# Performance work log

Measured on AMD Instinct MI355X. Metric: run time of the kernel, lower is better.

The kernel has to match this reference:

```python
import jax, jax.numpy as jnp
import numpy as np

# dims
B_, L_, DIN, H, DOUT, NL = 2, 1024, 512, 768, 512, 4
ED, N, K = H, 16, 4            # expand_factor=1 -> d_inner=H; d_state=16; d_conv=4
DTR = (H + 15) // 16           # dt_rank = ceil(d_model/16) = 48


def setup_inputs() -> dict:
    key = jax.random.key(0)
    ks = iter(jax.random.split(key, 32))
    def g(shape, s=0.02):
        return jax.random.normal(next(ks), shape, jnp.float32) * s
    inp = dict(
        x=jax.random.normal(next(ks), (B_, L_, DIN), jnp.float32),
        in_proj_w=g((H, DIN)), in_proj_b=jnp.zeros((H,), jnp.float32),
        out_proj_w=g((DOUT, H)), out_proj_b=jnp.zeros((DOUT,), jnp.float32),
        ln1_w=jnp.ones((NL, H), jnp.float32), ln1_b=jnp.zeros((NL, H), jnp.float32),
        ln2_w=jnp.ones((NL, H), jnp.float32), ln2_b=jnp.zeros((NL, H), jnp.float32),
        ffn_w1=g((NL, 4 * H, H)), ffn_b1=jnp.zeros((NL, 4 * H), jnp.float32),
        ffn_w2=g((NL, H, 4 * H)), ffn_b2=jnp.zeros((NL, H), jnp.float32),
        rms_w=jnp.ones((NL, ED), jnp.float32),
        m_in_w=g((NL, 2 * ED, H)),
        conv_w=g((NL, ED, 1, K), 0.2), conv_b=jnp.zeros((NL, ED), jnp.float32),
        xproj_w=g((NL, DTR + 2 * N, ED)),
        dt_w=g((NL, ED, DTR), 0.1), dt_b=g((NL, ED), 0.1),
        A_log=jnp.log(jnp.tile(jnp.arange(1, N + 1, dtype=jnp.float32), (NL, ED, 1))),
        Dp=jnp.ones((NL, ED), jnp.float32),
        m_out_w=g((NL, H, ED)),
    )
    return inp


def _layernorm(x, w, b):
    m = x.mean(-1, keepdims=True)
    v = ((x - m) ** 2).mean(-1, keepdims=True)
    return (x - m) / jnp.sqrt(v + 1e-5) * w + b


def _rmsnorm(x, w):
    return x * jax.lax.rsqrt((x * x).mean(-1, keepdims=True) + 1e-5) * w


def _selective_scan(dA, dBx):
    # h_t = dA_t * h_{t-1} + dBx_t, done as a parallel associative scan over L
    def comb(c1, c2):
        a1, b1 = c1
        a2, b2 = c2
        return a1 * a2, a2 * b1 + b2
    _, h = jax.lax.associative_scan(comb, (dA, dBx), axis=1)
    return h  # (B, L, ED, N)


def _mamba(x, rw, iw, cw, cb, xw, dw, db, Alog, Dp, ow):
    # mambapy ResidualBlock: x + MambaBlock(RMSNorm(x))
    xn = _rmsnorm(x, rw)
    xz = xn @ iw.T                             # (B, L, 2*ED)
    xi, z = jnp.split(xz, 2, axis=-1)
    # causal depthwise conv1d (padding = K-1 left)
    xc = jax.lax.conv_general_dilated(
        xi.transpose(0, 2, 1), cw, (1,), [(K - 1, 0)],
        feature_group_count=ED, dimension_numbers=('NCH', 'OIH', 'NCH'))
    xi = jax.nn.silu(xc.transpose(0, 2, 1) + cb)
    dbc = xi @ xw.T                            # (B, L, DTR + 2N)
    d = dbc[..., :DTR]
    Bm = dbc[..., DTR:DTR + N]
    Cm = dbc[..., DTR + N:]
    delta = jax.nn.softplus(d @ dw.T + db)     # (B, L, ED)
    A = -jnp.exp(Alog)                         # (ED, N)
    dA = jnp.exp(delta[..., None] * A)         # (B, L, ED, N)
    dBx = (delta * xi)[..., None] * Bm[:, :, None, :]
    h = _selective_scan(dA, dBx)
    y = jnp.einsum('blen,bln->ble', h, Cm) + Dp * xi
    y = y * jax.nn.silu(z)
    return x + y @ ow.T


def reference(x, in_proj_w, in_proj_b, out_proj_w, out_proj_b,
              ln1_w, ln1_b, ln2_w, ln2_b,
              ffn_w1, ffn_b1, ffn_w2, ffn_b2,
              rms_w, m_in_w, conv_w, conv_b, xproj_w,
              dt_w, dt_b, A_log, Dp, m_out_w):
    h = x @ in_proj_w.T + in_proj_b
    for i in range(NL):
        h = h + _mamba(_layernorm(h, ln1_w[i], ln1_b[i]),
                       rms_w[i], m_in_w[i], conv_w[i], conv_b[i], xproj_w[i],
                       dt_w[i], dt_b[i], A_log[i], Dp[i], m_out_w[i])
        hn = _layernorm(h, ln2_w[i], ln2_b[i])
        h = h + jax.nn.relu(hn @ ffn_w1[i].T + ffn_b1[i]) @ ffn_w2[i].T + ffn_b2[i]
    return h @ out_proj_w.T + out_proj_b
```

## Files before the change

### kernel.cpp

```cpp
#include <hip/hip_runtime.h>
#include <stdint.h>

typedef unsigned short u16;
typedef __attribute__((ext_vector_type(8))) short short8;
typedef __attribute__((ext_vector_type(4))) float f32x4;

static __device__ __forceinline__ u16 f2bf(float f){
  unsigned int x = __float_as_uint(f);
  unsigned int r = (x + 0x7FFFu + ((x >> 16) & 1u)) >> 16;
  return (u16)r;
}
static __device__ __forceinline__ float bf2f(u16 u){
  return __uint_as_float(((unsigned int)u) << 16);
}

__global__ __launch_bounds__(256) void prep_cvt(
    const float* __restrict__ s0, const float* __restrict__ s1,
    const float* __restrict__ s2, const float* __restrict__ s3,
    const float* __restrict__ s4, const float* __restrict__ s5,
    const float* __restrict__ s6,
    u16* __restrict__ d0, u16* __restrict__ d1, u16* __restrict__ d2,
    u16* __restrict__ d3, u16* __restrict__ d4, u16* __restrict__ d5,
    u16* __restrict__ d6){
  size_t i = ((size_t)blockIdx.x * 256 + threadIdx.x) * 4;
  const float* src; u16* dst; size_t base;
  if      (i <  1048576){ src = s0; dst = d0; base = 0; }
  else if (i <  1441792){ src = s1; dst = d1; base = 1048576; }
  else if (i <  1835008){ src = s2; dst = d2; base = 1441792; }
  else if (i <  6553600){ src = s3; dst = d3; base = 1835008; }
  else if (i <  8912896){ src = s4; dst = d4; base = 6553600; }
  else if (i < 18350080){ src = s5; dst = d5; base = 8912896; }
  else                  { src = s6; dst = d6; base = 18350080; }
  size_t o = i - base;
  float4 v = *reinterpret_cast<const float4*>(src + o);
  union { u16 u[4]; unsigned long long ll; } t;
  t.u[0] = f2bf(v.x); t.u[1] = f2bf(v.y); t.u[2] = f2bf(v.z); t.u[3] = f2bf(v.w);
  *reinterpret_cast<unsigned long long*>(dst + o) = t.ll;
}

__global__ __launch_bounds__(256) void build_dbc(const float* __restrict__ dt_w,
                                                 const float* __restrict__ xproj_w,
                                                 u16* __restrict__ out){
  const int total = 4 * 896 * 768;
  for (int idx = blockIdx.x * 256 + threadIdx.x; idx < total; idx += gridDim.x * 256){
    int l = idx / (896 * 768);
    int rem = idx - l * 896 * 768;
    int row = rem / 768;
    int k = rem - row * 768;
    float v = 0.f;
    if (row < 768){
      const float* dtr = dt_w + ((size_t)l * 768 + row) * 48;
      const float* xp  = xproj_w + (size_t)l * 80 * 768 + k;
      #pragma unroll 8
      for (int j = 0; j < 48; j++) v += dtr[j] * xp[(size_t)j * 768];
    } else if (row < 800){
      v = xproj_w[(size_t)l * 80 * 768 + (size_t)(48 + row - 768) * 768 + k];
    }
    out[idx] = f2bf(v);
  }
}

__global__ __launch_bounds__(256) void ln_rms_kernel(const float* __restrict__ in,
                                                     const float* __restrict__ w,
                                                     const float* __restrict__ b,
                                                     const float* __restrict__ rw,
                                                     float* __restrict__ xln,
                                                     u16* __restrict__ outB){
  int row = blockIdx.x;
  const float* x = in + (size_t)row * 768;
  int t = threadIdx.x;
  float v0 = x[t], v1 = x[t + 256], v2 = x[t + 512];
  float s = v0 + v1 + v2;
  float s2 = v0 * v0 + v1 * v1 + v2 * v2;
  #pragma unroll
  for (int off = 1; off < 64; off <<= 1){ s += __shfl_xor(s, off); s2 += __shfl_xor(s2, off); }
  __shared__ float red[8];
  int wid = t >> 6, lane = t & 63;
  if (lane == 0){ red[wid] = s; red[4 + wid] = s2; }
  __syncthreads();
  s = red[0] + red[1] + red[2] + red[3];
  s2 = red[4] + red[5] + red[6] + red[7];
  float mean = s * (1.f / 768.f);
  float var = s2 * (1.f / 768.f) - mean * mean;
  float rstd = rsqrtf(var + 1e-5f);
  float o0 = (v0 - mean) * rstd * w[t] + b[t];
  float o1 = (v1 - mean) * rstd * w[t + 256] + b[t + 256];
  float o2 = (v2 - mean) * rstd * w[t + 512] + b[t + 512];
  xln[(size_t)row * 768 + t]       = o0;
  xln[(size_t)row * 768 + t + 256] = o1;
  xln[(size_t)row * 768 + t + 512] = o2;
  float q = o0 * o0 + o1 * o1 + o2 * o2;
  #pragma unroll
  for (int off = 1; off < 64; off <<= 1){ q += __shfl_xor(q, off); }
  __syncthreads();
  if (lane == 0) red[wid] = q;
  __syncthreads();
  q = red[0] + red[1] + red[2] + red[3];
  float rs = rsqrtf(q * (1.f / 768.f) + 1e-5f);
  outB[(size_t)row * 768 + t]       = f2bf(o0 * rs * rw[t]);
  outB[(size_t)row * 768 + t + 256] = f2bf(o1 * rs * rw[t + 256]);
  outB[(size_t)row * 768 + t + 512] = f2bf(o2 * rs * rw[t + 512]);
}

__global__ __launch_bounds__(256) void ln_kernel(const float* __restrict__ in,
                                                 const float* __restrict__ w,
                                                 const float* __restrict__ b,
                                                 u16* __restrict__ outB){
  int row = blockIdx.x;
  const float* x = in + (size_t)row * 768;
  int t = threadIdx.x;
  float v0 = x[t], v1 = x[t + 256], v2 = x[t + 512];
  float s = v0 + v1 + v2;
  float s2 = v0 * v0 + v1 * v1 + v2 * v2;
  #pragma unroll
  for (int off = 1; off < 64; off <<= 1){ s += __shfl_xor(s, off); s2 += __shfl_xor(s2, off); }
  __shared__ float red[8];
  int wid = t >> 6, lane = t & 63;
  if (lane == 0){ red[wid] = s; red[4 + wid] = s2; }
  __syncthreads();
  s = red[0] + red[1] + red[2] + red[3];
  s2 = red[4] + red[5] + red[6] + red[7];
  float mean = s * (1.f / 768.f);
  float var = s2 * (1.f / 768.f) - mean * mean;
  float rstd = rsqrtf(var + 1e-5f);
  #pragma unroll
  for (int j = 0; j < 3; j++){
    int e = t + j * 256;
    float v = (j == 0) ? v0 : (j == 1) ? v1 : v2;
    outB[(size_t)row * 768 + e] = f2bf((v - mean) * rstd * w[e] + b[e]);
  }
}

__global__ __launch_bounds__(256) void conv_silu(const float* __restrict__ xz,
                                                 const float* __restrict__ cw,
                                                 const float* __restrict__ cb,
                                                 u16* __restrict__ xi){
  int row = blockIdx.x;
  int b = row >> 10, l = row & 1023;
  for (int e = threadIdx.x; e < 768; e += 256){
    const float* w = cw + (size_t)e * 4;
    float acc = cb[e];
    #pragma unroll
    for (int k = 0; k < 4; k++){
      int ls = l - 3 + k;
      if (ls >= 0) acc += w[k] * xz[((size_t)((b << 10) + ls)) * 1536 + e];
    }
    float sv = acc / (1.f + __expf(-acc));
    xi[(size_t)row * 768 + e] = f2bf(sv);
  }
}

__global__ __launch_bounds__(256) void scan_pass1(const float* __restrict__ delta,
                                                  const u16* __restrict__ xi,
                                                  const float* __restrict__ bc,
                                                  const float* __restrict__ A_log,
                                                  float* __restrict__ asum,
                                                  float* __restrict__ bsum){
  int bid = blockIdx.x;
  int eg = bid % 3; int c = (bid / 3) & 63; int b = bid / 192;
  int e = eg * 256 + threadIdx.x;
  float A[16], a[16], s[16];
  const float* al = A_log + (size_t)e * 16;
  #pragma unroll
  for (int n = 0; n < 16; n++){ A[n] = -__expf(al[n]); a[n] = 1.f; s[n] = 0.f; }
  for (int ll = 0; ll < 16; ll++){
    int row = b * 1024 + c * 16 + ll;
    float dlt = delta[(size_t)row * 768 + e];
    float xiv = bf2f(xi[(size_t)row * 768 + e]);
    float du = dlt * xiv;
    const float* bm = bc + (size_t)row * 32;
    #pragma unroll
    for (int n = 0; n < 16; n++){
      float dA = __expf(dlt * A[n]);
      s[n] = dA * s[n] + du * bm[n];
      a[n] *= dA;
    }
  }
  size_t base = (((size_t)(b * 64 + c) * 768) + e) * 16;
  #pragma unroll
  for (int n = 0; n < 16; n++){ asum[base + n] = a[n]; bsum[base + n] = s[n]; }
}

__global__ __launch_bounds__(256) void scan_pass2(const float* __restrict__ asum,
                                                  const float* __restrict__ bsum,
                                                  float* __restrict__ h0){
  int idx = blockIdx.x * 256 + threadIdx.x;
  int b = idx / 12288;
  int en = idx - b * 12288;
  float h = 0.f;
  for (int c = 0; c < 64; c++){
    size_t i = ((size_t)(b * 64 + c) * 12288) + en;
    h0[i] = h;
    h = asum[i] * h + bsum[i];
  }
}

__global__ __launch_bounds__(256) void scan_pass3(const float* __restrict__ delta,
                                                  const u16* __restrict__ xi,
                                                  const float* __restrict__ bc,
                                                  const float* __restrict__ A_log,
                                                  const float* __restrict__ h0,
                                                  const float* __restrict__ Dp,
                                                  const float* __restrict__ xz,
                                                  u16* __restrict__ y){
  int bid = blockIdx.x;
  int eg = bid % 3; int c = (bid / 3) & 63; int b = bid / 192;
  int e = eg * 256 + threadIdx.x;
  float A[16], s[16];
  const float* al = A_log + (size_t)e * 16;
  #pragma unroll
  for (int n = 0; n < 16; n++) A[n] = -__expf(al[n]);
  size_t base = (((size_t)(b * 64 + c) * 768) + e) * 16;
  #pragma unroll
  for (int n = 0; n < 16; n++) s[n] = h0[base + n];
  float dp = Dp[e];
  for (int ll = 0; ll < 16; ll++){
    int row = b * 1024 + c * 16 + ll;
    float dlt = delta[(size_t)row * 768 + e];
    float xiv = bf2f(xi[(size_t)row * 768 + e]);
    float du = dlt * xiv;
    const float* bm = bc + (size_t)row * 32;
    const float* cm = bm + 16;
    float acc = 0.f;
    #pragma unroll
    for (int n = 0; n < 16; n++){
      float dA = __expf(dlt * A[n]);
      s[n] = dA * s[n] + du * bm[n];
      acc += s[n] * cm[n];
    }
    float yv = acc + dp * xiv;
    float z = xz[(size_t)row * 1536 + 768 + e];
    yv *= z / (1.f + __expf(-z));
    y[(size_t)row * 768 + e] = f2bf(yv);
  }
}

template<int MODE>
__global__ __launch_bounds__(256, 2) void gemm128x64(
    const u16* __restrict__ A, const u16* __restrict__ Bw, int N, int Kd,
    float* __restrict__ outF, u16* __restrict__ outB,
    const float* __restrict__ bias, const float* __restrict__ r1,
    const float* __restrict__ r2,
    float* __restrict__ dl, float* __restrict__ bco, const float* __restrict__ dtb){
  __shared__ u16 sm[3][(128 + 64) * 64];
  const int tid = threadIdx.x;
  const int wid = tid >> 6, lane = tid & 63;
  const int lhi = lane >> 4, llo = lane & 15;
  const int wr = wid >> 1, wc = wid & 1;
  int nwg = (int)(gridDim.x * gridDim.y);
  int orig = (int)(blockIdx.y * gridDim.x + blockIdx.x);
  int wg = (orig & 7) * (nwg >> 3) + (orig >> 3);
  const int m0 = (wg & 15) * 128, n0 = (wg >> 4) * 64;
  const int nk = Kd >> 6;
  f32x4 acc[4][2] = {};

  auto stage = [&](int buf, int kt){
    const u16* Ab = A + (size_t)m0 * Kd + kt * 64;
    const u16* Bb = Bw + (size_t)n0 * Kd + kt * 64;
    u16* base = &sm[buf][0];
    #pragma unroll
    for (int j = 0; j < 4; j++){
      int sl = j * 256 + tid;
      int row = sl >> 3;
      int ch = (sl & 7) ^ (row & 7);
      __builtin_amdgcn_global_load_lds(
          (const __attribute__((address_space(1))) void*)(Ab + (size_t)row * Kd + ch * 8),
          (__attribute__((address_space(3))) void*)(base + sl * 8), 16, 0, 0);
    }
    #pragma unroll
    for (int j = 0; j < 2; j++){
      int sl = j * 256 + tid;
      int row = sl >> 3;
      int ch = (sl & 7) ^ (row & 7);
      __builtin_amdgcn_global_load_lds(
          (const __attribute__((address_space(1))) void*)(Bb + (size_t)row * Kd + ch * 8),
          (__attribute__((address_space(3))) void*)(base + 128 * 64 + sl * 8), 16, 0, 0);
    }
  };

  stage(0, 0);
  if (nk > 1) stage(1, 1);
  int bsel = 2;
  for (int kt = 0; kt < nk; ++kt){
    if (kt + 1 < nk){
      asm volatile("s_waitcnt vmcnt(6)" ::: "memory");
    } else {
      asm volatile("s_waitcnt vmcnt(0)" ::: "memory");
    }
    __builtin_amdgcn_s_barrier();
    __builtin_amdgcn_sched_barrier(0);
    if (kt + 2 < nk){
      stage(bsel, kt + 2);
      bsel = (bsel == 2) ? 0 : bsel + 1;
    }
    int cb = kt % 3;
    const u16* Asb = &sm[cb][0];
    const u16* Bsb = &sm[cb][128 * 64];
    short8 af[4][2], bfr[2][2];
    #pragma unroll
    for (int mi = 0; mi < 4; mi++){
      int row = wr * 64 + mi * 16 + llo;
      const u16* rp = Asb + row * 64;
      #pragma unroll
      for (int s2 = 0; s2 < 2; s2++){
        int ch = (s2 * 4 + lhi) ^ (row & 7);
        af[mi][s2] = *(const short8*)(rp + ch * 8);
      }
    }
    #pragma unroll
    for (int ni = 0; ni < 2; ni++){
      int row = wc * 32 + ni * 16 + llo;
      const u16* rp = Bsb + row * 64;
      #pragma unroll
      for (int s2 = 0; s2 < 2; s2++){
        int ch = (s2 * 4 + lhi) ^ (row & 7);
        bfr[ni][s2] = *(const short8*)(rp + ch * 8);
      }
    }
    #pragma unroll
    for (int s2 = 0; s2 < 2; s2++)
      #pragma unroll
      for (int mi = 0; mi < 4; mi++)
        #pragma unroll
        for (int ni = 0; ni < 2; ni++)
          acc[mi][ni] = __builtin_amdgcn_mfma_f32_16x16x32_bf16(
              af[mi][s2], bfr[ni][s2], acc[mi][ni], 0, 0, 0);
  }
  #pragma unroll
  for (int mi = 0; mi < 4; mi++){
    #pragma unroll
    for (int ni = 0; ni < 2; ni++){
      int r0 = m0 + wr * 64 + mi * 16 + lhi * 4;
      int c = n0 + wc * 32 + ni * 16 + llo;
      #pragma unroll
      for (int r = 0; r < 4; r++){
        int rr = r0 + r;
        float v = acc[mi][ni][r];
        if (MODE == 0){
          size_t idx = (size_t)rr * N + c;
          if (bias) v += bias[c];
          if (r1) v += r1[idx];
          if (r2) v += r2[idx];
          outF[idx] = v;
          if (outB) outB[idx] = f2bf(v);
        } else if (MODE == 1){
          size_t idx = (size_t)rr * N + c;
          v += bias[c];
          outB[idx] = f2bf(v > 0.f ? v : 0.f);
        } else {
          if (c < 768){
            float tv = v + dtb[c];
            dl[(size_t)rr * 768 + c] = (tv > 20.f) ? tv : log1pf(__expf(tv));
          } else if (c < 800){
            bco[(size_t)rr * 32 + (c - 768)] = v;
          }
        }
      }
    }
  }
}

extern "C" void kernel_launch(void* const* d_in, const int* in_sizes, int n_in,
                              void* d_out, int out_size, void* d_ws, size_t ws_size,
                              hipStream_t stream){
  (void)in_sizes; (void)n_in; (void)out_size; (void)ws_size;
  const float* x_f       = (const float*)d_in[0];
  const float* in_proj_w = (const float*)d_in[1];
  const float* in_proj_b = (const float*)d_in[2];
  const float* out_proj_w= (const float*)d_in[3];
  const float* out_proj_b= (const float*)d_in[4];
  const float* ln1_w     = (const float*)d_in[5];
  const float* ln1_b     = (const float*)d_in[6];
  const float* ln2_w     = (const float*)d_in[7];
  const float* ln2_b     = (const float*)d_in[8];
  const float* ffn_w1    = (const float*)d_in[9];
  const float* ffn_b1    = (const float*)d_in[10];
  const float* ffn_w2    = (const float*)d_in[11];
  const float* ffn_b2    = (const float*)d_in[12];
  const float* rms_w     = (const float*)d_in[13];
  const float* m_in_w    = (const float*)d_in[14];
  const float* conv_w    = (const float*)d_in[15];
  const float* conv_b    = (const float*)d_in[16];
  const float* xproj_w   = (const float*)d_in[17];
  const float* dt_w      = (const float*)d_in[18];
  const float* dt_b      = (const float*)d_in[19];
  const float* A_log     = (const float*)d_in[20];
  const float* Dp        = (const float*)d_in[21];
  const float* m_out_w   = (const float*)d_in[22];

  char* ws = (char*)d_ws;
  size_t off = 0;
  auto alloc = [&](size_t bytes) -> char* {
    char* p = ws + off;
    off += (bytes + 255) & ~(size_t)255;
    return p;
  };
  u16* wb_inp  = (u16*)alloc((size_t)768 * 512 * 2);
  u16* wb_outp = (u16*)alloc((size_t)512 * 768 * 2);
  u16* wb_min  = (u16*)alloc((size_t)4 * 1536 * 768 * 2);
  u16* wb_mout = (u16*)alloc((size_t)4 * 768 * 768 * 2);
  u16* wb_f1   = (u16*)alloc((size_t)4 * 3072 * 768 * 2);
  u16* wb_f2   = (u16*)alloc((size_t)4 * 768 * 3072 * 2);
  u16* wb_dbc  = (u16*)alloc((size_t)4 * 896 * 768 * 2);
  u16* xbf     = (u16*)alloc((size_t)2048 * 512 * 2);
  float* hA    = (float*)alloc((size_t)2048 * 768 * 4);
  float* hB    = (float*)alloc((size_t)2048 * 768 * 4);
  float* xln   = (float*)alloc((size_t)2048 * 768 * 4);
  u16* xnbf    = (u16*)alloc((size_t)2048 * 768 * 2);
  float* xz    = (float*)alloc((size_t)2048 * 1536 * 4);
  u16* xibf    = (u16*)alloc((size_t)2048 * 768 * 2);
  float* dltb  = (float*)alloc((size_t)2048 * 768 * 4);
  float* bcb   = (float*)alloc((size_t)2048 * 32 * 4);
  float* asum  = (float*)alloc((size_t)2 * 64 * 768 * 16 * 4);
  float* bsum  = (float*)alloc((size_t)2 * 64 * 768 * 16 * 4);
  float* h0    = (float*)alloc((size_t)2 * 64 * 768 * 16 * 4);
  u16* ybf     = (u16*)alloc((size_t)2048 * 768 * 2);
  u16* tbf     = (u16*)alloc((size_t)2048 * 768 * 2);
  u16* f1bf    = (u16*)alloc((size_t)2048 * 3072 * 2);
  u16* hfbf    = (u16*)alloc((size_t)2048 * 768 * 2);

  prep_cvt<<<27136, 256, 0, stream>>>(x_f, in_proj_w, out_proj_w, m_in_w,
                                      m_out_w, ffn_w1, ffn_w2,
                                      xbf, wb_inp, wb_outp, wb_min,
                                      wb_mout, wb_f1, wb_f2);
  build_dbc<<<2048, 256, 0, stream>>>(dt_w, xproj_w, wb_dbc);

  auto gemm = [&](int mode, const u16* Ain, const u16* Bww, int N, int K,
                  float* oF, u16* oB, const float* bias, const float* rr1,
                  const float* rr2, float* dl, float* bco, const float* dtb){
    dim3 g(16, N / 64), blk(256);
    if (mode == 0)
      gemm128x64<0><<<g, blk, 0, stream>>>(Ain, Bww, N, K, oF, oB, bias, rr1, rr2, dl, bco, dtb);
    else if (mode == 1)
      gemm128x64<1><<<g, blk, 0, stream>>>(Ain, Bww, N, K, oF, oB, bias, rr1, rr2, dl, bco, dtb);
    else
      gemm128x64<2><<<g, blk, 0, stream>>>(Ain, Bww, N, K, oF, oB, bias, rr1, rr2, dl, bco, dtb);
  };

  gemm(0, xbf, wb_inp, 768, 512, hA, nullptr, in_proj_b, nullptr, nullptr,
       nullptr, nullptr, nullptr);

  for (int i = 0; i < 4; i++){
    ln_rms_kernel<<<2048, 256, 0, stream>>>(hA, ln1_w + i * 768, ln1_b + i * 768,
                                            rms_w + i * 768, xln, xnbf);
    gemm(0, xnbf, wb_min + (size_t)i * 1536 * 768, 1536, 768, xz, nullptr,
         nullptr, nullptr, nullptr, nullptr, nullptr, nullptr);
    conv_silu<<<2048, 256, 0, stream>>>(xz, conv_w + (size_t)i * 768 * 4,
                                        conv_b + i * 768, xibf);
    gemm(2, xibf, wb_dbc + (size_t)i * 896 * 768, 896, 768, nullptr, nullptr,
         nullptr, nullptr, nullptr, dltb, bcb, dt_b + i * 768);
    scan_pass1<<<384, 256, 0, stream>>>(dltb, xibf, bcb,
                                        A_log + (size_t)i * 768 * 16, asum, bsum);
    scan_pass2<<<96, 256, 0, stream>>>(asum, bsum, h0);
    scan_pass3<<<384, 256, 0, stream>>>(dltb, xibf, bcb,
                                        A_log + (size_t)i * 768 * 16, h0,
                                        Dp + i * 768, xz, ybf);
    gemm(0, ybf, wb_mout + (size_t)i * 768 * 768, 768, 768, hB, nullptr,
         nullptr, hA, xln, nullptr, nullptr, nullptr);
    ln_kernel<<<2048, 256, 0, stream>>>(hB, ln2_w + i * 768, ln2_b + i * 768, tbf);
    gemm(1, tbf, wb_f1 + (size_t)i * 3072 * 768, 3072, 768, nullptr, f1bf,
         ffn_b1 + i * 3072, nullptr, nullptr, nullptr, nullptr, nullptr);
    gemm(0, f1bf, wb_f2 + (size_t)i * 768 * 3072, 768, 3072, hA,
         (i == 3) ? hfbf : nullptr, ffn_b2 + i * 768, hB, nullptr,
         nullptr, nullptr, nullptr);
  }
  gemm(0, hfbf, wb_outp, 512, 768, (float*)d_out, nullptr, out_proj_b,
       nullptr, nullptr, nullptr, nullptr, nullptr);
}
```

Baseline: 725.9 us.

## Retile GEMMs, store xz in bf16, precompute silu(z), coarsen scan chunks

The GEMM is templated on tile size. Most projections move from 128x64 tiles to 64x64 tiles with a 4-deep LDS pipeline, doubling the grid, while FFN1 uses 128x128 tiles. The in-projection now writes bf16 instead of fp32. conv_silu computes silu(z) once into a bf16 buffer, so the scan reads fewer bytes. The scan uses 32-step chunks with interleaved float2 a/b sums, halving the sequential chunk count in pass 2, and prep_cvt converts 8 elements per thread. In exchange, more values are rounded to bf16 and the scan passes launch fewer blocks.

```diff
diff --git a/kernel.cpp b/kernel.cpp
--- a/kernel.cpp
+++ b/kernel.cpp
@@ -22,7 +22,7 @@
     u16* __restrict__ d0, u16* __restrict__ d1, u16* __restrict__ d2,
     u16* __restrict__ d3, u16* __restrict__ d4, u16* __restrict__ d5,
     u16* __restrict__ d6){
-  size_t i = ((size_t)blockIdx.x * 256 + threadIdx.x) * 4;
+  size_t i = ((size_t)blockIdx.x * 256 + threadIdx.x) * 8;
   const float* src; u16* dst; size_t base;
   if      (i <  1048576){ src = s0; dst = d0; base = 0; }
   else if (i <  1441792){ src = s1; dst = d1; base = 1048576; }
@@ -32,10 +32,13 @@
   else if (i < 18350080){ src = s5; dst = d5; base = 8912896; }
   else                  { src = s6; dst = d6; base = 18350080; }
   size_t o = i - base;
-  float4 v = *reinterpret_cast<const float4*>(src + o);
-  union { u16 u[4]; unsigned long long ll; } t;
-  t.u[0] = f2bf(v.x); t.u[1] = f2bf(v.y); t.u[2] = f2bf(v.z); t.u[3] = f2bf(v.w);
-  *reinterpret_cast<unsigned long long*>(dst + o) = t.ll;
+  #pragma unroll
+  for (int p = 0; p < 2; p++){
+    float4 v = *reinterpret_cast<const float4*>(src + o + p * 4);
+    union { u16 u[4]; unsigned long long ll; } t;
+    t.u[0] = f2bf(v.x); t.u[1] = f2bf(v.y); t.u[2] = f2bf(v.z); t.u[3] = f2bf(v.w);
+    *reinterpret_cast<unsigned long long*>(dst + o + p * 4) = t.ll;
+  }
 }
 
 __global__ __launch_bounds__(256) void build_dbc(const float* __restrict__ dt_w,
@@ -131,10 +134,11 @@
   }
 }
 
-__global__ __launch_bounds__(256) void conv_silu(const float* __restrict__ xz,
+__global__ __launch_bounds__(256) void conv_silu(const u16* __restrict__ xzb,
                                                  const float* __restrict__ cw,
                                                  const float* __restrict__ cb,
-                                                 u16* __restrict__ xi){
+                                                 u16* __restrict__ xi,
+                                                 u16* __restrict__ zs){
   int row = blockIdx.x;
   int b = row >> 10, l = row & 1023;
   for (int e = threadIdx.x; e < 768; e += 256){
@@ -143,10 +147,12 @@
     #pragma unroll
     for (int k = 0; k < 4; k++){
       int ls = l - 3 + k;
-      if (ls >= 0) acc += w[k] * xz[((size_t)((b << 10) + ls)) * 1536 + e];
+      if (ls >= 0) acc += w[k] * bf2f(xzb[((size_t)((b << 10) + ls)) * 1536 + e]);
     }
     float sv = acc / (1.f + __expf(-acc));
     xi[(size_t)row * 768 + e] = f2bf(sv);
+    float z = bf2f(xzb[(size_t)row * 1536 + 768 + e]);
+    zs[(size_t)row * 768 + e] = f2bf(z / (1.f + __expf(-z)));
   }
 }
 
@@ -154,17 +160,16 @@
                                                   const u16* __restrict__ xi,
                                                   const float* __restrict__ bc,
                                                   const float* __restrict__ A_log,
-                                                  float* __restrict__ asum,
-                                                  float* __restrict__ bsum){
+                                                  float2* __restrict__ ab){
   int bid = blockIdx.x;
-  int eg = bid % 3; int c = (bid / 3) & 63; int b = bid / 192;
+  int eg = bid % 3; int c = (bid / 3) & 31; int b = bid / 96;
   int e = eg * 256 + threadIdx.x;
   float A[16], a[16], s[16];
   const float* al = A_log + (size_t)e * 16;
   #pragma unroll
   for (int n = 0; n < 16; n++){ A[n] = -__expf(al[n]); a[n] = 1.f; s[n] = 0.f; }
-  for (int ll = 0; ll < 16; ll++){
-    int row = b * 1024 + c * 16 + ll;
+  for (int ll = 0; ll < 32; ll++){
+    int row = b * 1024 + c * 32 + ll;
     float dlt = delta[(size_t)row * 768 + e];
     float xiv = bf2f(xi[(size_t)row * 768 + e]);
     float du = dlt * xiv;
@@ -176,22 +181,22 @@
       a[n] *= dA;
     }
   }
-  size_t base = (((size_t)(b * 64 + c) * 768) + e) * 16;
-  #pragma unroll
-  for (int n = 0; n < 16; n++){ asum[base + n] = a[n]; bsum[base + n] = s[n]; }
-}
-
-__global__ __launch_bounds__(256) void scan_pass2(const float* __restrict__ asum,
-                                                  const float* __restrict__ bsum,
+  size_t base = (((size_t)(b * 32 + c) * 768) + e) * 16;
+  #pragma unroll
+  for (int n = 0; n < 16; n++){ ab[base + n] = make_float2(a[n], s[n]); }
+}
+
+__global__ __launch_bounds__(128) void scan_pass2(const float2* __restrict__ ab,
                                                   float* __restrict__ h0){
-  int idx = blockIdx.x * 256 + threadIdx.x;
+  int idx = blockIdx.x * 128 + threadIdx.x;
   int b = idx / 12288;
   int en = idx - b * 12288;
   float h = 0.f;
-  for (int c = 0; c < 64; c++){
-    size_t i = ((size_t)(b * 64 + c) * 12288) + en;
+  for (int c = 0; c < 32; c++){
+    size_t i = ((size_t)(b * 32 + c) * 12288) + en;
     h0[i] = h;
-    h = asum[i] * h + bsum[i];
+    float2 v = ab[i];
+    h = v.x * h + v.y;
   }
 }
 
@@ -201,21 +206,21 @@
                                                   const float* __restrict__ A_log,
                                                   const float* __restrict__ h0,
                                                   const float* __restrict__ Dp,
-                                                  const float* __restrict__ xz,
+                                                  const u16* __restrict__ zs,
                                                   u16* __restrict__ y){
   int bid = blockIdx.x;
-  int eg = bid % 3; int c = (bid / 3) & 63; int b = bid / 192;
+  int eg = bid % 3; int c = (bid / 3) & 31; int b = bid / 96;
   int e = eg * 256 + threadIdx.x;
   float A[16], s[16];
   const float* al = A_log + (size_t)e * 16;
   #pragma unroll
   for (int n = 0; n < 16; n++) A[n] = -__expf(al[n]);
-  size_t base = (((size_t)(b * 64 + c) * 768) + e) * 16;
+  size_t base = (((size_t)(b * 32 + c) * 768) + e) * 16;
   #pragma unroll
   for (int n = 0; n < 16; n++) s[n] = h0[base + n];
   float dp = Dp[e];
-  for (int ll = 0; ll < 16; ll++){
-    int row = b * 1024 + c * 16 + ll;
+  for (int ll = 0; ll < 32; ll++){
+    int row = b * 1024 + c * 32 + ll;
     float dlt = delta[(size_t)row * 768 + e];
     float xiv = bf2f(xi[(size_t)row * 768 + e]);
     float du = dlt * xiv;
@@ -229,77 +234,79 @@
       acc += s[n] * cm[n];
     }
     float yv = acc + dp * xiv;
-    float z = xz[(size_t)row * 1536 + 768 + e];
-    yv *= z / (1.f + __expf(-z));
+    yv *= bf2f(zs[(size_t)row * 768 + e]);
     y[(size_t)row * 768 + e] = f2bf(yv);
   }
 }
 
-template<int MODE>
-__global__ __launch_bounds__(256, 2) void gemm128x64(
+template<int MODE, int TS>
+__global__ __launch_bounds__(256, 2) void gemmT(
     const u16* __restrict__ A, const u16* __restrict__ Bw, int N, int Kd,
     float* __restrict__ outF, u16* __restrict__ outB,
     const float* __restrict__ bias, const float* __restrict__ r1,
     const float* __restrict__ r2,
     float* __restrict__ dl, float* __restrict__ bco, const float* __restrict__ dtb){
-  __shared__ u16 sm[3][(128 + 64) * 64];
+  constexpr int NBUF = (TS == 64) ? 4 : 3;
+  constexpr int DEPTH = NBUF - 1;
+  constexpr int MI = TS / 32;
+  __shared__ u16 sm[NBUF][2 * TS * 64];
   const int tid = threadIdx.x;
   const int wid = tid >> 6, lane = tid & 63;
   const int lhi = lane >> 4, llo = lane & 15;
-  const int wr = wid >> 1, wc = wid & 1;
+  const int wm = (wid >> 1) * (TS / 2), wn = (wid & 1) * (TS / 2);
   int nwg = (int)(gridDim.x * gridDim.y);
   int orig = (int)(blockIdx.y * gridDim.x + blockIdx.x);
   int wg = (orig & 7) * (nwg >> 3) + (orig >> 3);
-  const int m0 = (wg & 15) * 128, n0 = (wg >> 4) * 64;
+  int gx = (int)gridDim.x;
+  int bx = wg % gx, by = wg / gx;
+  const int m0 = bx * TS, n0 = by * TS;
   const int nk = Kd >> 6;
-  f32x4 acc[4][2] = {};
+  f32x4 acc[MI][MI] = {};
 
   auto stage = [&](int buf, int kt){
     const u16* Ab = A + (size_t)m0 * Kd + kt * 64;
     const u16* Bb = Bw + (size_t)n0 * Kd + kt * 64;
-    u16* base = &sm[buf][0];
-    #pragma unroll
-    for (int j = 0; j < 4; j++){
+    u16* basep = &sm[buf][0];
+    #pragma unroll
+    for (int j = 0; j < TS / 32; j++){
       int sl = j * 256 + tid;
       int row = sl >> 3;
       int ch = (sl & 7) ^ (row & 7);
       __builtin_amdgcn_global_load_lds(
           (const __attribute__((address_space(1))) void*)(Ab + (size_t)row * Kd + ch * 8),
-          (__attribute__((address_space(3))) void*)(base + sl * 8), 16, 0, 0);
-    }
-    #pragma unroll
-    for (int j = 0; j < 2; j++){
+          (__attribute__((address_space(3))) void*)(basep + sl * 8), 16, 0, 0);
+    }
+    #pragma unroll
+    for (int j = 0; j < TS / 32; j++){
       int sl = j * 256 + tid;
       int row = sl >> 3;
       int ch = (sl & 7) ^ (row & 7);
       __builtin_amdgcn_global_load_lds(
           (const __attribute__((address_space(1))) void*)(Bb + (size_t)row * Kd + ch * 8),
-          (__attribute__((address_space(3))) void*)(base + 128 * 64 + sl * 8), 16, 0, 0);
+          (__attribute__((address_space(3))) void*)(basep + TS * 64 + sl * 8), 16, 0, 0);
     }
   };
 
-  stage(0, 0);
-  if (nk > 1) stage(1, 1);
-  int bsel = 2;
+  #pragma unroll
+  for (int t = 0; t < DEPTH; t++) stage(t, t);
   for (int kt = 0; kt < nk; ++kt){
-    if (kt + 1 < nk){
-      asm volatile("s_waitcnt vmcnt(6)" ::: "memory");
+    if constexpr (TS == 64){
+      if (kt + 2 < nk)      asm volatile("s_waitcnt vmcnt(8)" ::: "memory");
+      else if (kt + 1 < nk) asm volatile("s_waitcnt vmcnt(4)" ::: "memory");
+      else                  asm volatile("s_waitcnt vmcnt(0)" ::: "memory");
     } else {
-      asm volatile("s_waitcnt vmcnt(0)" ::: "memory");
+      if (kt + 1 < nk)      asm volatile("s_waitcnt vmcnt(8)" ::: "memory");
+      else                  asm volatile("s_waitcnt vmcnt(0)" ::: "memory");
     }
     __builtin_amdgcn_s_barrier();
     __builtin_amdgcn_sched_barrier(0);
-    if (kt + 2 < nk){
-      stage(bsel, kt + 2);
-      bsel = (bsel == 2) ? 0 : bsel + 1;
-    }
-    int cb = kt % 3;
-    const u16* Asb = &sm[cb][0];
-    const u16* Bsb = &sm[cb][128 * 64];
-    short8 af[4][2], bfr[2][2];
-    #pragma unroll
-    for (int mi = 0; mi < 4; mi++){
-      int row = wr * 64 + mi * 16 + llo;
+    if (kt + DEPTH < nk) stage((kt + DEPTH) % NBUF, kt + DEPTH);
+    const u16* Asb = &sm[kt % NBUF][0];
+    const u16* Bsb = &sm[kt % NBUF][TS * 64];
+    short8 af[MI][2], bfr[MI][2];
+    #pragma unroll
+    for (int mi = 0; mi < MI; mi++){
+      int row = wm + mi * 16 + llo;
       const u16* rp = Asb + row * 64;
       #pragma unroll
       for (int s2 = 0; s2 < 2; s2++){
@@ -308,8 +315,8 @@
       }
     }
     #pragma unroll
-    for (int ni = 0; ni < 2; ni++){
-      int row = wc * 32 + ni * 16 + llo;
+    for (int ni = 0; ni < MI; ni++){
+      int row = wn + ni * 16 + llo;
       const u16* rp = Bsb + row * 64;
       #pragma unroll
       for (int s2 = 0; s2 < 2; s2++){
@@ -320,18 +327,18 @@
     #pragma unroll
     for (int s2 = 0; s2 < 2; s2++)
       #pragma unroll
-      for (int mi = 0; mi < 4; mi++)
+      for (int mi = 0; mi < MI; mi++)
         #pragma unroll
-        for (int ni = 0; ni < 2; ni++)
+        for (int ni = 0; ni < MI; ni++)
           acc[mi][ni] = __builtin_amdgcn_mfma_f32_16x16x32_bf16(
               af[mi][s2], bfr[ni][s2], acc[mi][ni], 0, 0, 0);
   }
   #pragma unroll
-  for (int mi = 0; mi < 4; mi++){
-    #pragma unroll
-    for (int ni = 0; ni < 2; ni++){
-      int r0 = m0 + wr * 64 + mi * 16 + lhi * 4;
-      int c = n0 + wc * 32 + ni * 16 + llo;
+  for (int mi = 0; mi < MI; mi++){
+    #pragma unroll
+    for (int ni = 0; ni < MI; ni++){
+      int r0 = m0 + wm + mi * 16 + lhi * 4;
+      int c = n0 + wn + ni * 16 + llo;
       #pragma unroll
       for (int r = 0; r < 4; r++){
         int rr = r0 + r;
@@ -347,6 +354,8 @@
           size_t idx = (size_t)rr * N + c;
           v += bias[c];
           outB[idx] = f2bf(v > 0.f ? v : 0.f);
+        } else if (MODE == 3){
+          outB[(size_t)rr * N + c] = f2bf(v);
         } else {
           if (c < 768){
             float tv = v + dtb[c];
@@ -407,63 +416,67 @@
   float* hB    = (float*)alloc((size_t)2048 * 768 * 4);
   float* xln   = (float*)alloc((size_t)2048 * 768 * 4);
   u16* xnbf    = (u16*)alloc((size_t)2048 * 768 * 2);
-  float* xz    = (float*)alloc((size_t)2048 * 1536 * 4);
+  u16* xzb     = (u16*)alloc((size_t)2048 * 1536 * 2);
   u16* xibf    = (u16*)alloc((size_t)2048 * 768 * 2);
+  u16* zsbf    = (u16*)alloc((size_t)2048 * 768 * 2);
   float* dltb  = (float*)alloc((size_t)2048 * 768 * 4);
   float* bcb   = (float*)alloc((size_t)2048 * 32 * 4);
-  float* asum  = (float*)alloc((size_t)2 * 64 * 768 * 16 * 4);
-  float* bsum  = (float*)alloc((size_t)2 * 64 * 768 * 16 * 4);
-  float* h0    = (float*)alloc((size_t)2 * 64 * 768 * 16 * 4);
+  float2* ab   = (float2*)alloc((size_t)2 * 32 * 768 * 16 * 8);
+  float* h0    = (float*)alloc((size_t)2 * 32 * 768 * 16 * 4);
   u16* ybf     = (u16*)alloc((size_t)2048 * 768 * 2);
   u16* tbf     = (u16*)alloc((size_t)2048 * 768 * 2);
   u16* f1bf    = (u16*)alloc((size_t)2048 * 3072 * 2);
   u16* hfbf    = (u16*)alloc((size_t)2048 * 768 * 2);
 
-  prep_cvt<<<27136, 256, 0, stream>>>(x_f, in_proj_w, out_proj_w, m_in_w,
+  prep_cvt<<<13568, 256, 0, stream>>>(x_f, in_proj_w, out_proj_w, m_in_w,
                                       m_out_w, ffn_w1, ffn_w2,
                                       xbf, wb_inp, wb_outp, wb_min,
                                       wb_mout, wb_f1, wb_f2);
   build_dbc<<<2048, 256, 0, stream>>>(dt_w, xproj_w, wb_dbc);
 
-  auto gemm = [&](int mode, const u16* Ain, const u16* Bww, int N, int K,
-                  float* oF, u16* oB, const float* bias, const float* rr1,
-                  const float* rr2, float* dl, float* bco, const float* dtb){
-    dim3 g(16, N / 64), blk(256);
+  auto gemm64 = [&](int mode, const u16* Ain, const u16* Bww, int N, int K,
+                    float* oF, u16* oB, const float* bias, const float* rr1,
+                    const float* rr2, float* dl, float* bco, const float* dtb){
+    dim3 g(32, N / 64), blk(256);
     if (mode == 0)
-      gemm128x64<0><<<g, blk, 0, stream>>>(Ain, Bww, N, K, oF, oB, bias, rr1, rr2, dl, bco, dtb);
-    else if (mode == 1)
-      gemm128x64<1><<<g, blk, 0, stream>>>(Ain, Bww, N, K, oF, oB, bias, rr1, rr2, dl, bco, dtb);
+      gemmT<0,64><<<g, blk, 0, stream>>>(Ain, Bww, N, K, oF, oB, bias, rr1, rr2, dl, bco, dtb);
+    else if (mode == 2)
+      gemmT<2,64><<<g, blk, 0, stream>>>(Ain, Bww, N, K, oF, oB, bias, rr1, rr2, dl, bco, dtb);
     else
-      gemm128x64<2><<<g, blk, 0, stream>>>(Ain, Bww, N, K, oF, oB, bias, rr1, rr2, dl, bco, dtb);
+      gemmT<3,64><<<g, blk, 0, stream>>>(Ain, Bww, N, K, oF, oB, bias, rr1, rr2, dl, bco, dtb);
   };
 
-  gemm(0, xbf, wb_inp, 768, 512, hA, nullptr, in_proj_b, nullptr, nullptr,
-       nullptr, nullptr, nullptr);
+  gemm64(0, xbf, wb_inp, 768, 512, hA, nullptr, in_proj_b, nullptr, nullptr,
+         nullptr, nullptr, nullptr);
 
   for (int i = 0; i < 4; i++){
     ln_rms_kernel<<<2048, 256, 0, stream>>>(hA, ln1_w + i * 768, ln1_b + i * 768,
                                             rms_w + i * 768, xln, xnbf);
-    gemm(0, xnbf, wb_min + (size_t)i * 1536 * 768, 1536, 768, xz, nullptr,
-         nullptr, nullptr, nullptr, nullptr, nullptr, nullptr);
-    conv_silu<<<2048, 256, 0, stream>>>(xz, conv_w + (size_t)i * 768 * 4,
-                                        conv_b + i * 768, xibf);
-    gemm(2, xibf, wb_dbc + (size_t)i * 896 * 768, 896, 768, nullptr, nullptr,
-         nullptr, nullptr, nullptr, dltb, bcb, dt_b + i * 768);
-    scan_pass1<<<384, 256, 0, stream>>>(dltb, xibf, bcb,
-                                        A_log + (size_t)i * 768 * 16, asum, bsum);
-    scan_pass2<<<96, 256, 0, stream>>>(asum, bsum, h0);
-    scan_pass3<<<384, 256, 0, stream>>>(dltb, xibf, bcb,
+    gemm64(3, xnbf, wb_min + (size_t)i * 1536 * 768, 1536, 768, nullptr, xzb,
+           nullptr, nullptr, nullptr, nullptr, nullptr, nullptr);
+    conv_silu<<<2048, 256, 0, stream>>>(xzb, conv_w + (size_t)i * 768 * 4,
+                                        conv_b + i * 768, xibf, zsbf);
+    gemm64(2, xibf, wb_dbc + (size_t)i * 896 * 768, 896, 768, nullptr, nullptr,
+           nullptr, nullptr, nullptr, dltb, bcb, dt_b + i * 768);
+    scan_pass1<<<192, 256, 0, stream>>>(dltb, xibf, bcb,
+                                        A_log + (size_t)i * 768 * 16, ab);
+    scan_pass2<<<192, 128, 0, stream>>>(ab, h0);
+    scan_pass3<<<192, 256, 0, stream>>>(dltb, xibf, bcb,
                                         A_log + (size_t)i * 768 * 16, h0,
-                                        Dp + i * 768, xz, ybf);
-    gemm(0, ybf, wb_mout + (size_t)i * 768 * 768, 768, 768, hB, nullptr,
-         nullptr, hA, xln, nullptr, nullptr, nullptr);
+                                        Dp + i * 768, zsbf, ybf);
+    gemm64(0, ybf, wb_mout + (size_t)i * 768 * 768, 768, 768, hB, nullptr,
+           nullptr, hA, xln, nullptr, nullptr, nullptr);
     ln_kernel<<<2048, 256, 0, stream>>>(hB, ln2_w + i * 768, ln2_b + i * 768, tbf);
-    gemm(1, tbf, wb_f1 + (size_t)i * 3072 * 768, 3072, 768, nullptr, f1bf,
-         ffn_b1 + i * 3072, nullptr, nullptr, nullptr, nullptr, nullptr);
-    gemm(0, f1bf, wb_f2 + (size_t)i * 768 * 3072, 768, 3072, hA,
-         (i == 3) ? hfbf : nullptr, ffn_b2 + i * 768, hB, nullptr,
-         nullptr, nullptr, nullptr);
-  }
-  gemm(0, hfbf, wb_outp, 512, 768, (float*)d_out, nullptr, out_proj_b,
-       nullptr, nullptr, nullptr, nullptr, nullptr);
-}
+    {
+      dim3 g(16, 3072 / 128), blk(256);
+      gemmT<1,128><<<g, blk, 0, stream>>>(tbf, wb_f1 + (size_t)i * 3072 * 768, 3072, 768,
+                                          nullptr, f1bf, ffn_b1 + i * 3072, nullptr,
+                                          nullptr, nullptr, nullptr, nullptr);
+    }
+    gemm64(0, f1bf, wb_f2 + (size_t)i * 768 * 3072, 768, 3072, hA,
+           (i == 3) ? hfbf : nullptr, ffn_b2 + i * 768, hB, nullptr,
+           nullptr, nullptr, nullptr);
+  }
+  gemm64(0, hfbf, wb_outp, 512, 768, (float*)d_out, nullptr, out_proj_b,
+         nullptr, nullptr, nullptr, nullptr, nullptr);
+}
```

New measurement: 716.6 us. About the same (-1.3%).
